# Optimization experiments

Measured on AMD Instinct MI355X. Metric: run time of the kernel, lower is better.

## Reference

```python
import jax, jax.numpy as jnp
import numpy as np

N_HEADS = 16
D_K = 64
DIM = 1024
NEG = -1e12
LN_EPS = 1e-5


def setup_inputs() -> dict:
    key = jax.random.key(0)
    ks = jax.random.split(key, 8)
    B, S, D = 2, 2048, DIM
    H, K = N_HEADS, D_K
    f = lambda k, shp: jax.random.normal(k, shp, dtype=jnp.float32)
    scale = 0.02
    return {
        "input_Q": f(ks[0], (B, S, D)),
        "input_K": f(ks[1], (B, S, D)),
        "input_V": f(ks[2], (B, S, D)),
        "attention_mask": jax.random.randint(ks[3], (B, S), 0, 2, dtype=jnp.int32),
        "W_Q": f(ks[4], (H * K, D)) * scale,  # nn.Linear weight layout [out, in]
        "W_K": f(ks[5], (H * K, D)) * scale,
        "W_V": f(ks[6], (H * K, D)) * scale,
        "W_O": f(ks[7], (D, H * K)) * scale,
        "gamma": jnp.ones((D,), jnp.float32),
        "beta": jnp.zeros((D,), jnp.float32),
    }


def reference(input_Q, input_K, input_V, attention_mask, W_Q, W_K, W_V, W_O, gamma, beta):
    B, S, D = input_Q.shape

    def proj(x, W):  # [B,S,D] @ [HK,D]^T -> [B,H,S,K]
        return (x @ W.T).reshape(B, S, N_HEADS, D_K).transpose(0, 2, 1, 3)

    Q = proj(input_Q, W_Q)
    K = proj(input_K, W_K)
    V = proj(input_V, W_V)

    scores = jnp.einsum('bhqk,bhsk->bhqs', Q, K) / np.float32(np.sqrt(D_K))

    # Faithful reproduction of scores_mask (including its inverted-looking logic):
    # mask = clamp(padding_mask + strict_upper_tri - 1, min=0); scores += (1-mask)*NEG
    am = attention_mask.astype(scores.dtype)[:, None, None, :]          # [B,1,1,S]
    low_tri = jnp.triu(jnp.ones((S, S), scores.dtype), k=1)             # 1 - tril(ones)
    m = jnp.maximum(am + low_tri - 1.0, 0.0)
    scores = scores + (1.0 - m) * NEG

    attn = jax.nn.softmax(scores, axis=-1)
    ctx = jnp.einsum('bhqs,bhsk->bhqk', attn, V)                        # [B,H,S,K]
    ctx = ctx.transpose(0, 2, 1, 3).reshape(B, S, N_HEADS * D_K)

    out = ctx @ W_O.T + input_Q                                         # fc + residual
    mu = jnp.mean(out, axis=-1, keepdims=True)
    var = jnp.var(out, axis=-1, keepdims=True)
    return (out - mu) / jnp.sqrt(var + LN_EPS) * gamma + beta
```

## Files before the change

### kernel.cpp

```cpp
#include <hip/hip_runtime.h>

#define NH    16
#define DK    64
#define DIM   1024
#define BATCH 2
#define SEQ   2048
#define MROWS (BATCH*SEQ)
#define QSCALE 0.18033688011112043f
#define SENT   -44.0f
#define PCONST 5.684341886080802e-14f

typedef unsigned short bfraw;
typedef __attribute__((ext_vector_type(8))) __bf16 bf16x8;
typedef __attribute__((ext_vector_type(4))) __bf16 bf16x4;
typedef __attribute__((ext_vector_type(8))) unsigned short u16x8;
typedef __attribute__((ext_vector_type(4))) unsigned short u16x4;
typedef __attribute__((ext_vector_type(4))) short s16x4;
typedef __attribute__((ext_vector_type(4))) float f32x4;

__device__ __forceinline__ float bf2f(bfraw u) {
    union { unsigned int i; float f; } x; x.i = ((unsigned int)u) << 16; return x.f;
}
__device__ __forceinline__ bfraw f2bf(float f) {
    union { float f; unsigned int i; } x; x.f = f;
    unsigned int r = x.i + 0x7FFFu + ((x.i >> 16) & 1u);
    return (bfraw)(r >> 16);
}
__device__ __forceinline__ float fexp2(float x) {
#if __has_builtin(__builtin_amdgcn_exp2f)
    return __builtin_amdgcn_exp2f(x);
#else
    return exp2f(x);
#endif
}

__device__ __forceinline__ f32x4 mfma16(s16x4 a, s16x4 b, f32x4 c) {
#if __has_builtin(__builtin_amdgcn_mfma_f32_16x16x16_bf16)
    union { s16x4 s; bf16x4 h; } ua, ub; ua.s = a; ub.s = b;
    return __builtin_amdgcn_mfma_f32_16x16x16_bf16(ua.h, ub.h, c, 0, 0, 0);
#elif __has_builtin(__builtin_amdgcn_mfma_f32_16x16x16bf16_1k)
    return __builtin_amdgcn_mfma_f32_16x16x16bf16_1k(a, b, c, 0, 0, 0);
#else
    asm("v_mfma_f32_16x16x16_bf16 %0, %1, %2, %0" : "+v"(c) : "v"(a), "v"(b));
    return c;
#endif
}

__device__ __forceinline__ float block_reduce(float val, float* rbuf, int op) {
    const int lane = threadIdx.x & 63, wave = threadIdx.x >> 6;
    #pragma unroll
    for (int off = 32; off; off >>= 1) {
        float o = __shfl_xor(val, off, 64);
        val = op ? (val + o) : fmaxf(val, o);
    }
    if (lane == 0) rbuf[wave] = val;
    __syncthreads();
    float r = op ? (rbuf[0] + rbuf[1] + rbuf[2] + rbuf[3])
                 : fmaxf(fmaxf(rbuf[0], rbuf[1]), fmaxf(rbuf[2], rbuf[3]));
    __syncthreads();
    return r;
}

__global__ __launch_bounds__(256) void cvt_kernel(
        const float* __restrict__ x0, const float* __restrict__ x1, const float* __restrict__ x2,
        const float* __restrict__ w0, const float* __restrict__ w1, const float* __restrict__ w2,
        const float* __restrict__ w3, bfraw* __restrict__ Xb, bfraw* __restrict__ Wb) {
    const int t = blockIdx.y;
    const float* src; bfraw* dst; int n;
    if (t < 3) { src = (t == 0) ? x0 : (t == 1) ? x1 : x2; dst = Xb + t * (MROWS * DIM); n = MROWS * DIM; }
    else { int u = t - 3; src = (u == 0) ? w0 : (u == 1) ? w1 : (u == 2) ? w2 : w3;
           dst = Wb + u * (DIM * DIM); n = DIM * DIM; }
    int idx = (blockIdx.x * 256 + threadIdx.x) * 8;
    if (idx >= n) return;
    f32x4 a = *(const f32x4*)(src + idx);
    f32x4 b = *(const f32x4*)(src + idx + 4);
    u16x8 o;
    #pragma unroll
    for (int j = 0; j < 4; j++) { o[j] = f2bf(a[j]); o[4 + j] = f2bf(b[j]); }
    *(u16x8*)(dst + idx) = o;
}

__device__ __forceinline__ void gemm128(const bfraw* __restrict__ A, const bfraw* __restrict__ B,
                                        int m0, int n0, f32x4 acc[4][4]) {
    __shared__ __align__(16) bfraw As[2][128 * 64];
    __shared__ __align__(16) bfraw Bs[2][128 * 64];
    const int tid = threadIdx.x, wave = tid >> 6;
    const int lane = tid & 63, lrow = lane & 15, quad = lane >> 4;
    const int wy = wave >> 1, wx = wave & 1;
    const int swz = lrow & 7;
    const int srow = tid >> 2;
    const int cg0  = (tid & 3) << 1;
    const int gc   = cg0 << 3;
    const int e7   = srow & 7;
    const int o0 = ((cg0 ^ e7) << 3), o1 = (((cg0 | 1) ^ e7) << 3);

    const bfraw* pa0 = A + (m0 + srow) * DIM + gc;
    const bfraw* pa1 = A + (m0 + 64 + srow) * DIM + gc;
    const bfraw* pb0 = B + (n0 + srow) * DIM + gc;
    const bfraw* pb1 = B + (n0 + 64 + srow) * DIM + gc;

    #pragma unroll
    for (int i = 0; i < 4; i++)
        #pragma unroll
        for (int j = 0; j < 4; j++) { f32x4 z = {0.f, 0.f, 0.f, 0.f}; acc[i][j] = z; }

    u16x8 ha0[4], hb0[4], ha1[4], hb1[4];

    auto LOAD = [&](u16x8 ha[4], u16x8 hb[4], int kk) {
        ha[0] = *(const u16x8*)(pa0 + kk);     ha[1] = *(const u16x8*)(pa0 + kk + 8);
        ha[2] = *(const u16x8*)(pa1 + kk);     ha[3] = *(const u16x8*)(pa1 + kk + 8);
        hb[0] = *(const u16x8*)(pb0 + kk);     hb[1] = *(const u16x8*)(pb0 + kk + 8);
        hb[2] = *(const u16x8*)(pb1 + kk);     hb[3] = *(const u16x8*)(pb1 + kk + 8);
    };
    auto STORE = [&](bfraw* Ad, bfraw* Bd, u16x8 ha[4], u16x8 hb[4]) {
        *(u16x8*)&Ad[srow * 64 + o0]        = ha[0];
        *(u16x8*)&Ad[srow * 64 + o1]        = ha[1];
        *(u16x8*)&Ad[(64 + srow) * 64 + o0] = ha[2];
        *(u16x8*)&Ad[(64 + srow) * 64 + o1] = ha[3];
        *(u16x8*)&Bd[srow * 64 + o0]        = hb[0];
        *(u16x8*)&Bd[srow * 64 + o1]        = hb[1];
        *(u16x8*)&Bd[(64 + srow) * 64 + o0] = hb[2];
        *(u16x8*)&Bd[(64 + srow) * 64 + o1] = hb[3];
    };
    auto COMPUTE = [&](const bfraw* Ad, const bfraw* Bd) {
        #pragma unroll
        for (int ks = 0; ks < 2; ks++) {
            const int c = (ks << 2) | quad;
            bf16x8 af[4], bfg[4];
            #pragma unroll
            for (int mi = 0; mi < 4; mi++)
                af[mi] = *(const bf16x8*)&Ad[(wy * 64 + mi * 16 + lrow) * 64 + ((c ^ swz) << 3)];
            #pragma unroll
            for (int ni = 0; ni < 4; ni++)
                bfg[ni] = *(const bf16x8*)&Bd[(wx * 64 + ni * 16 + lrow) * 64 + ((c ^ swz) << 3)];
            #pragma unroll
            for (int mi = 0; mi < 4; mi++)
                #pragma unroll
                for (int ni = 0; ni < 4; ni++)
                    acc[mi][ni] = __builtin_amdgcn_mfma_f32_16x16x32_bf16(af[mi], bfg[ni], acc[mi][ni], 0, 0, 0);
        }
    };

    LOAD(ha0, hb0, 0);
    LOAD(ha1, hb1, 64);

    #pragma unroll
    for (int m2 = 0; m2 < DIM / 128; m2++) {
        const int k0 = m2 * 128;
        STORE(As[0], Bs[0], ha0, hb0);
        if (k0 + 128 < DIM) LOAD(ha0, hb0, k0 + 128);
        __syncthreads();
        COMPUTE(As[0], Bs[0]);
        STORE(As[1], Bs[1], ha1, hb1);
        if (k0 + 192 < DIM) LOAD(ha1, hb1, k0 + 192);
        __syncthreads();
        COMPUTE(As[1], Bs[1]);
    }
}

__global__ __launch_bounds__(256) void qkv_gemm(
        const bfraw* __restrict__ Xb, const bfraw* __restrict__ Wb,
        bfraw* __restrict__ Qp, bfraw* __restrict__ Kp, bfraw* __restrict__ Vt) {
    const int which = blockIdx.z;
    const bfraw* A = Xb + which * (MROWS * DIM);
    const bfraw* B = Wb + which * (DIM * DIM);
    bfraw* O = (which == 0) ? Qp : (which == 1) ? Kp : Vt;
    const int m0 = blockIdx.x * 128, n0 = blockIdx.y * 128;
    f32x4 acc[4][4];
    gemm128(A, B, m0, n0, acc);
    const int lane = threadIdx.x & 63, wave = threadIdx.x >> 6;
    const int lrow = lane & 15, quad = lane >> 4;
    const int wy = wave >> 1, wx = wave & 1;
    const float scale = (which == 0) ? QSCALE : 1.0f;
    #pragma unroll
    for (int mi = 0; mi < 4; mi++)
        #pragma unroll
        for (int ni = 0; ni < 4; ni++)
            #pragma unroll
            for (int i = 0; i < 4; i++) {
                int m = m0 + wy * 64 + mi * 16 + quad * 4 + i;
                int n = n0 + wx * 64 + ni * 16 + lrow;
                int b = m >> 11, s = m & (SEQ - 1), h = n >> 6, kk = n & (DK - 1);
                bfraw v = f2bf(acc[mi][ni][i] * scale);
                if (which == 2) O[(((b * NH + h) * DK) + kk) * SEQ + s] = v;
                else            O[(((b * NH + h) * SEQ) + s) * DK + kk] = v;
            }
}

template<bool NEAR>
__device__ __forceinline__ void qk_soft(
        const bfraw* Kb, const bf16x8 qf[2], const float* Mkf,
        int kt0, int lrow, int quad, int q_ln, float& lsum, s16x4 pb[4]) {
    #pragma unroll
    for (int n = 0; n < 4; n++) {
        const int srow = n * 16 + lrow;
        bf16x8 kfa = *(const bf16x8*)&Kb[srow * 64 + ((quad ^ (lrow & 7)) << 3)];
        bf16x8 kfb = *(const bf16x8*)&Kb[srow * 64 + (((4 | quad) ^ (lrow & 7)) << 3)];
        f32x4 z = {0.f, 0.f, 0.f, 0.f};
        z = __builtin_amdgcn_mfma_f32_16x16x32_bf16(kfa, qf[0], z, 0, 0, 0);
        z = __builtin_amdgcn_mfma_f32_16x16x32_bf16(kfb, qf[1], z, 0, 0, 0);
        f32x4 mv = *(const f32x4*)&Mkf[kt0 + n * 16 + quad * 4];
        union { bf16x4 h; s16x4 s; } pk;
        #pragma unroll
        for (int i = 0; i < 4; i++) {
            float m = mv[i];
            if (NEAR) { int s = kt0 + n * 16 + quad * 4 + i; m = (s > q_ln) ? m : 0.0f; }
            float p = fexp2(fmaf(m, z[i] - SENT, SENT));
            lsum += p;
            pk.h[i] = (__bf16)p;
        }
        pb[n] = pk.s;
    }
}

__global__ __launch_bounds__(512) void attn_flash(
        const bfraw* __restrict__ Qp, const bfraw* __restrict__ Kp, const bfraw* __restrict__ Vt,
        const int* __restrict__ mask, bfraw* __restrict__ Ctx) {
    __shared__ __align__(16) bfraw Ks[2][64 * 64];
    __shared__ __align__(16) bfraw Vs[2][64 * 64];
    __shared__ float Mkf[SEQ];
    __shared__ float Ps[8][64];
    __shared__ float Scol[64];
    const int bh = blockIdx.x, yy = blockIdx.y;
    const int gg = yy >> 3, jj = yy & 7;
    const int qt = gg ? (15 - jj) : jj;
    const int b = bh >> 4, h = bh & 15;
    const int tid = threadIdx.x, wave = tid >> 6, lane = tid & 63;
    const int lrow = lane & 15, quad = lane >> 4;
    const int baseK = ((b * NH + h) * SEQ) * DK;
    const int baseV = ((b * NH + h) * DK) * SEQ;
    const int qbase = qt * 128 + wave * 16;
    const int q_ln  = qbase + lrow;
    const int diagKt = qt * 128;
    const int ldr = tid >> 3;
    const int c8  = tid & 7;
    const int ldc = c8 << 3;
    const int cl  = ((c8 ^ (ldr & 7)) << 3);

    const int d_v = tid & 63, part = tid >> 6;
    float pacc = 0.f;
    {
        const bfraw* vrow = Vt + baseV + d_v * SEQ;
        for (int s0 = part * 8; s0 < diagKt; s0 += 64) {
            u16x8 v = *(const u16x8*)(vrow + s0);
            #pragma unroll
            for (int e = 0; e < 8; e++) pacc += bf2f(v[e]);
        }
    }
    for (int i = tid; i < SEQ; i += 512) Mkf[i] = (mask[b * SEQ + i] != 0) ? 1.0f : 0.0f;
    Ps[part][d_v] = pacc;
    __syncthreads();
    if (tid < 64) {
        float sc = 0.f;
        #pragma unroll
        for (int p = 0; p < 8; p++) sc += Ps[p][tid];
        Scol[tid] = sc;
    }
    __syncthreads();

    bf16x8 qf[2];
    qf[0] = *(const bf16x8*)(Qp + baseK + q_ln * DK + quad * 8);
    qf[1] = *(const bf16x8*)(Qp + baseK + q_ln * DK + 32 + quad * 8);

    f32x4 Oa[4];
    #pragma unroll
    for (int nd = 0; nd < 4; nd++)
        #pragma unroll
        for (int i = 0; i < 4; i++)
            Oa[nd][i] = PCONST * Scol[nd * 16 + quad * 4 + i];
    float lsum = 0.f;

    const int nt = (SEQ - diagKt) >> 6;
    int kt0 = diagKt;
    u16x8 k0 = *(const u16x8*)(Kp + baseK + (kt0 + ldr) * DK + ldc);
    u16x8 v0 = *(const u16x8*)(Vt + baseV + ldr * SEQ + kt0 + ldc);

    for (int t = 0; t < nt; t++, kt0 += 64) {
        bfraw* Kb = Ks[t & 1];
        bfraw* Vb = Vs[t & 1];
        *(u16x8*)&Kb[ldr * 64 + cl] = k0;
        *(u16x8*)&Vb[ldr * 64 + cl] = v0;
        if (t + 1 < nt) {
            const int kn = kt0 + 64;
            k0 = *(const u16x8*)(Kp + baseK + (kn + ldr) * DK + ldc);
            v0 = *(const u16x8*)(Vt + baseV + ldr * SEQ + kn + ldc);
        }
        __syncthreads();

        s16x4 pb[4];
        if (t < 2) qk_soft<true >(Kb, qf, Mkf, kt0, lrow, quad, q_ln, lsum, pb);
        else       qk_soft<false>(Kb, qf, Mkf, kt0, lrow, quad, q_ln, lsum, pb);

        #pragma unroll
        for (int nd = 0; nd < 4; nd++) {
            const int d = nd * 16 + lrow;
            #pragma unroll
            for (int sc = 0; sc < 4; sc++) {
                s16x4 vf = *(const s16x4*)&Vb[d * 64
                    + ((((sc << 1) | (quad >> 1)) ^ (d & 7)) << 3) + ((quad & 1) << 2)];
                Oa[nd] = mfma16(vf, pb[sc], Oa[nd]);
            }
        }
    }

    float r = lsum;
    r += __shfl_xor(r, 16, 64);
    r += __shfl_xor(r, 32, 64);
    const float inv = 1.0f / (r + (float)diagKt * PCONST);
    #pragma unroll
    for (int nd = 0; nd < 4; nd++) {
        u16x4 o;
        #pragma unroll
        for (int i = 0; i < 4; i++) o[i] = f2bf(Oa[nd][i] * inv);
        *(u16x4*)&Ctx[(b * SEQ + q_ln) * DIM + h * DK + nd * 16 + quad * 4] = o;
    }
}

__global__ __launch_bounds__(256) void out_gemm(
        const bfraw* __restrict__ Ctx, const bfraw* __restrict__ WoB, float* __restrict__ C) {
    const int m0 = blockIdx.x * 128, n0 = blockIdx.y * 128;
    f32x4 acc[4][4];
    gemm128(Ctx, WoB, m0, n0, acc);
    const int lane = threadIdx.x & 63, wave = threadIdx.x >> 6;
    const int lrow = lane & 15, quad = lane >> 4;
    const int wy = wave >> 1, wx = wave & 1;
    #pragma unroll
    for (int mi = 0; mi < 4; mi++)
        #pragma unroll
        for (int ni = 0; ni < 4; ni++)
            #pragma unroll
            for (int i = 0; i < 4; i++) {
                int m = m0 + wy * 64 + mi * 16 + quad * 4 + i;
                int n = n0 + wx * 64 + ni * 16 + lrow;
                C[m * DIM + n] = acc[mi][ni][i];
            }
}

__global__ __launch_bounds__(256) void ln_kernel(
        const float* __restrict__ C, const float* __restrict__ Xq,
        const float* __restrict__ gamma, const float* __restrict__ beta,
        float* __restrict__ out) {
    __shared__ float rbuf[4];
    const int m = blockIdx.x, tid = threadIdx.x;
    const float* crow = C + m * DIM;
    const float* xrow = Xq + m * DIM;
    float v[4]; float s = 0.f, s2 = 0.f;
    #pragma unroll
    for (int i = 0; i < 4; i++) {
        int d = tid + (i << 8);
        float x = crow[d] + xrow[d];
        v[i] = x; s += x; s2 += x * x;
    }
    float S  = block_reduce(s,  rbuf, 1);
    float S2 = block_reduce(s2, rbuf, 1);
    float mu  = S * (1.0f / DIM);
    float var = S2 * (1.0f / DIM) - mu * mu;
    float rstd = rsqrtf(var + 1e-5f);
    #pragma unroll
    for (int i = 0; i < 4; i++) {
        int d = tid + (i << 8);
        out[m * DIM + d] = (v[i] - mu) * rstd * gamma[d] + beta[d];
    }
}

extern "C" void kernel_launch(void* const* d_in, const int* in_sizes, int n_in,
                              void* d_out, int out_size, void* d_ws, size_t ws_size,
                              hipStream_t stream) {
    const float* Xq    = (const float*)d_in[0];
    const float* Xk    = (const float*)d_in[1];
    const float* Xv    = (const float*)d_in[2];
    const int*   mask  = (const int*)  d_in[3];
    const float* Wq    = (const float*)d_in[4];
    const float* Wk    = (const float*)d_in[5];
    const float* Wv    = (const float*)d_in[6];
    const float* Wo    = (const float*)d_in[7];
    const float* gamma = (const float*)d_in[8];
    const float* beta  = (const float*)d_in[9];
    float* out = (float*)d_out;

    char* ws = (char*)d_ws;
    bfraw* Xb   = (bfraw*)(ws);
    bfraw* Wb   = (bfraw*)(ws + (24u << 20));
    bfraw* Qp   = (bfraw*)(ws + (32u << 20));
    bfraw* Kp   = (bfraw*)(ws + (40u << 20));
    bfraw* Vt   = (bfraw*)(ws + (48u << 20));
    bfraw* Ctx  = (bfraw*)(ws + (56u << 20));
    float* C    = (float*)(ws);

    dim3 blk(256);
    cvt_kernel<<<dim3(MROWS * DIM / (256 * 8), 7), blk, 0, stream>>>(Xq, Xk, Xv, Wq, Wk, Wv, Wo, Xb, Wb);
    qkv_gemm  <<<dim3(MROWS / 128, DIM / 128, 3),  blk, 0, stream>>>(Xb, Wb, Qp, Kp, Vt);
    attn_flash<<<dim3(BATCH * NH, SEQ / 128),      dim3(512), 0, stream>>>(Qp, Kp, Vt, mask, Ctx);
    out_gemm  <<<dim3(MROWS / 128, DIM / 128),     blk, 0, stream>>>(Ctx, Wb + 3 * (DIM * DIM), C);
    ln_kernel <<<dim3(MROWS),                      blk, 0, stream>>>(C, Xq, gamma, beta, out);
}
```

Measured before the change: 214.1 us.

## Widen attention key tiles to 128 and fold mask into MFMA accumulator init

The flash attention loop now processes 128 keys per iteration instead of 64, doubling the shared K/V tile sizes and halving the number of barriers and loop iterations. The key mask is stored as an additive bias (0 or sentinel) and loaded as the MFMA accumulator's initial value, which removes the per-element fma before exp2. In exchange, shared memory use and register pressure from the larger pb and prefetch arrays both grow, which may lower occupancy. The masking now adds the query-key score onto the sentinel instead of multiplying by a 0/1 mask, so masked entries become exp2(sentinel + score) rather than exactly exp2(sentinel).

```diff
diff --git a/kernel.cpp b/kernel.cpp
--- a/kernel.cpp
+++ b/kernel.cpp
@@ -189,23 +189,22 @@
 
 template<bool NEAR>
 __device__ __forceinline__ void qk_soft(
-        const bfraw* Kb, const bf16x8 qf[2], const float* Mkf,
-        int kt0, int lrow, int quad, int q_ln, float& lsum, s16x4 pb[4]) {
-    #pragma unroll
-    for (int n = 0; n < 4; n++) {
+        const bfraw* Kb, const bf16x8 qf[2], const float* Mkb,
+        int kt0, int lrow, int quad, int q_ln, float& lsum, s16x4 pb[8]) {
+    #pragma unroll
+    for (int n = 0; n < 8; n++) {
         const int srow = n * 16 + lrow;
         bf16x8 kfa = *(const bf16x8*)&Kb[srow * 64 + ((quad ^ (lrow & 7)) << 3)];
         bf16x8 kfb = *(const bf16x8*)&Kb[srow * 64 + (((4 | quad) ^ (lrow & 7)) << 3)];
-        f32x4 z = {0.f, 0.f, 0.f, 0.f};
+        f32x4 z = *(const f32x4*)&Mkb[kt0 + n * 16 + quad * 4];
         z = __builtin_amdgcn_mfma_f32_16x16x32_bf16(kfa, qf[0], z, 0, 0, 0);
         z = __builtin_amdgcn_mfma_f32_16x16x32_bf16(kfb, qf[1], z, 0, 0, 0);
-        f32x4 mv = *(const f32x4*)&Mkf[kt0 + n * 16 + quad * 4];
         union { bf16x4 h; s16x4 s; } pk;
         #pragma unroll
         for (int i = 0; i < 4; i++) {
-            float m = mv[i];
-            if (NEAR) { int s = kt0 + n * 16 + quad * 4 + i; m = (s > q_ln) ? m : 0.0f; }
-            float p = fexp2(fmaf(m, z[i] - SENT, SENT));
+            float zz = z[i];
+            if (NEAR) { int s = kt0 + n * 16 + quad * 4 + i; zz = (s > q_ln) ? zz : SENT; }
+            float p = fexp2(zz);
             lsum += p;
             pk.h[i] = (__bf16)p;
         }
@@ -216,9 +215,9 @@
 __global__ __launch_bounds__(512) void attn_flash(
         const bfraw* __restrict__ Qp, const bfraw* __restrict__ Kp, const bfraw* __restrict__ Vt,
         const int* __restrict__ mask, bfraw* __restrict__ Ctx) {
-    __shared__ __align__(16) bfraw Ks[2][64 * 64];
-    __shared__ __align__(16) bfraw Vs[2][64 * 64];
-    __shared__ float Mkf[SEQ];
+    __shared__ __align__(16) bfraw Ks[2][128 * 64];
+    __shared__ __align__(16) bfraw Vs[2][64 * 128];
+    __shared__ float Mkb[SEQ];
     __shared__ float Ps[8][64];
     __shared__ float Scol[64];
     const int bh = blockIdx.x, yy = blockIdx.y;
@@ -232,10 +231,11 @@
     const int qbase = qt * 128 + wave * 16;
     const int q_ln  = qbase + lrow;
     const int diagKt = qt * 128;
-    const int ldr = tid >> 3;
-    const int c8  = tid & 7;
-    const int ldc = c8 << 3;
-    const int cl  = ((c8 ^ (ldr & 7)) << 3);
+    const int r8 = tid >> 3;
+    const int c8 = tid & 7;
+    const int kslot = (c8 ^ (r8 & 7)) << 3;
+    const int vslot0 = (c8 ^ (r8 & 7)) << 3;
+    const int vslot1 = ((8 | (c8 ^ (r8 & 7)))) << 3;
 
     const int d_v = tid & 63, part = tid >> 6;
     float pacc = 0.f;
@@ -247,7 +247,7 @@
             for (int e = 0; e < 8; e++) pacc += bf2f(v[e]);
         }
     }
-    for (int i = tid; i < SEQ; i += 512) Mkf[i] = (mask[b * SEQ + i] != 0) ? 1.0f : 0.0f;
+    for (int i = tid; i < SEQ; i += 512) Mkb[i] = (mask[b * SEQ + i] != 0) ? 0.0f : SENT;
     Ps[part][d_v] = pacc;
     __syncthreads();
     if (tid < 64) {
@@ -270,34 +270,41 @@
             Oa[nd][i] = PCONST * Scol[nd * 16 + quad * 4 + i];
     float lsum = 0.f;
 
-    const int nt = (SEQ - diagKt) >> 6;
+    const int nt = (SEQ - diagKt) >> 7;
     int kt0 = diagKt;
-    u16x8 k0 = *(const u16x8*)(Kp + baseK + (kt0 + ldr) * DK + ldc);
-    u16x8 v0 = *(const u16x8*)(Vt + baseV + ldr * SEQ + kt0 + ldc);
-
-    for (int t = 0; t < nt; t++, kt0 += 64) {
+    u16x8 k0 = *(const u16x8*)(Kp + baseK + (kt0 + r8) * DK + c8 * 8);
+    u16x8 k1 = *(const u16x8*)(Kp + baseK + (kt0 + 64 + r8) * DK + c8 * 8);
+    u16x8 v0 = *(const u16x8*)(Vt + baseV + r8 * SEQ + kt0 + c8 * 8);
+    u16x8 v1 = *(const u16x8*)(Vt + baseV + r8 * SEQ + kt0 + 64 + c8 * 8);
+
+    for (int t = 0; t < nt; t++, kt0 += 128) {
         bfraw* Kb = Ks[t & 1];
         bfraw* Vb = Vs[t & 1];
-        *(u16x8*)&Kb[ldr * 64 + cl] = k0;
-        *(u16x8*)&Vb[ldr * 64 + cl] = v0;
+        *(u16x8*)&Kb[r8 * 64 + kslot]        = k0;
+        *(u16x8*)&Kb[(64 + r8) * 64 + kslot] = k1;
+        *(u16x8*)&Vb[r8 * 128 + vslot0]      = v0;
+        *(u16x8*)&Vb[r8 * 128 + vslot1]      = v1;
         if (t + 1 < nt) {
-            const int kn = kt0 + 64;
-            k0 = *(const u16x8*)(Kp + baseK + (kn + ldr) * DK + ldc);
-            v0 = *(const u16x8*)(Vt + baseV + ldr * SEQ + kn + ldc);
+            const int kn = kt0 + 128;
+            k0 = *(const u16x8*)(Kp + baseK + (kn + r8) * DK + c8 * 8);
+            k1 = *(const u16x8*)(Kp + baseK + (kn + 64 + r8) * DK + c8 * 8);
+            v0 = *(const u16x8*)(Vt + baseV + r8 * SEQ + kn + c8 * 8);
+            v1 = *(const u16x8*)(Vt + baseV + r8 * SEQ + kn + 64 + c8 * 8);
         }
         __syncthreads();
 
-        s16x4 pb[4];
-        if (t < 2) qk_soft<true >(Kb, qf, Mkf, kt0, lrow, quad, q_ln, lsum, pb);
-        else       qk_soft<false>(Kb, qf, Mkf, kt0, lrow, quad, q_ln, lsum, pb);
+        s16x4 pb[8];
+        if (t == 0) qk_soft<true >(Kb, qf, Mkb, kt0, lrow, quad, q_ln, lsum, pb);
+        else        qk_soft<false>(Kb, qf, Mkb, kt0, lrow, quad, q_ln, lsum, pb);
 
         #pragma unroll
         for (int nd = 0; nd < 4; nd++) {
             const int d = nd * 16 + lrow;
             #pragma unroll
-            for (int sc = 0; sc < 4; sc++) {
-                s16x4 vf = *(const s16x4*)&Vb[d * 64
-                    + ((((sc << 1) | (quad >> 1)) ^ (d & 7)) << 3) + ((quad & 1) << 2)];
+            for (int sc = 0; sc < 8; sc++) {
+                const int ch = (sc << 1) | (quad >> 1);
+                const int slot = (ch & 8) | ((ch & 7) ^ (d & 7));
+                s16x4 vf = *(const s16x4*)&Vb[d * 128 + (slot << 3) + ((quad & 1) << 2)];
                 Oa[nd] = mfma16(vf, pb[sc], Oa[nd]);
             }
         }
```

Result: no change. 212.7 us (median of 2 runs) (-0.7%).
